# Optimization experiments

Measured on AMD Instinct MI355X. Metric: run time of the kernel, lower is better.

Reference implementation:

```python
import jax, jax.numpy as jnp
import numpy as np
import math

K_HEADS = 16  # nb_heads from init_kwargs


def setup_inputs() -> dict:
    key = jax.random.key(0)
    ks = jax.random.split(key, 7)
    B, M, H, D = 2, 2048, 1024, 1024 // K_HEADS
    return {
        "h": jax.random.normal(ks[0], (B, M, H), jnp.float32),
        "h_cache": jax.random.normal(ks[1], (B, M, H), jnp.float32),
        "key_pe": jax.random.normal(ks[2], (1, D, M), jnp.float32),
        "Wq": jax.random.normal(ks[3], (H, H), jnp.float32) * 0.02,
        "Wk": jax.random.normal(ks[4], (H, H), jnp.float32) * 0.02,
        "Wv": jax.random.normal(ks[5], (H, H), jnp.float32) * 0.02,
        "Wo": jax.random.normal(ks[6], (H, H), jnp.float32) * 0.02,
    }


def _heads(x, K):
    # [B, M, H] -> [B, K, M, D]
    B, M, H = x.shape
    return x.reshape(B, M, K, H // K).transpose(0, 2, 1, 3)


def reference(h, h_cache, key_pe, Wq, Wk, Wv, Wo):
    B, M, H = h.shape
    K = K_HEADS
    D = H // K
    q = _heads(h @ Wq.T, K)        # [B, K, M, D]
    k = _heads(h_cache @ Wk.T, K)  # [B, K, L, D], L == M
    v = _heads(h_cache @ Wv.T, K)  # [B, K, L, D]

    attn_cont = jnp.einsum("bkmd,bkld->bkml", q, k)            # content scores
    attn_pos = jnp.einsum("bkmd,dl->bkml", q, key_pe[0])       # positional scores
    attn = (attn_cont + attn_pos[..., :M]) / math.sqrt(D)
    attn = jax.nn.softmax(attn, axis=-1)  # computed as in source, but source
    # (faithfully) multiplies VALUE by attn_cont, not attn:
    out = jnp.einsum("bkml,bkld->bkmd", attn_cont, v)          # [B, K, M, D]
    out = out.transpose(0, 2, 1, 3).reshape(B, M, H)
    return out @ Wo.T
```

## Files before the change

kernel.cpp:

```cpp
#include <hip/hip_runtime.h>
#include <hip/hip_bf16.h>

#define BB 2
#define MM 2048
#define HH 1024
#define KH 16

typedef short s16x8 __attribute__((ext_vector_type(8)));
typedef float f32x4 __attribute__((ext_vector_type(4)));
typedef float f32x16 __attribute__((ext_vector_type(16)));

#define GLOBAL_AS __attribute__((address_space(1)))
#define LDS_AS    __attribute__((address_space(3)))

__device__ __forceinline__ void async_copy16(const void* g, void* l) {
    __builtin_amdgcn_global_load_lds((const GLOBAL_AS void*)g, (LDS_AS void*)l, 16, 0, 0);
}

struct __align__(8) bf16x4_t { __hip_bfloat16 x, y, z, w; };

__global__ __launch_bounds__(256) void cvt7(
    const float* __restrict__ s0, const float* __restrict__ s1,
    const float* __restrict__ s2, const float* __restrict__ s3,
    const float* __restrict__ s4, const float* __restrict__ s5,
    __hip_bfloat16* __restrict__ d0, __hip_bfloat16* __restrict__ d1,
    __hip_bfloat16* __restrict__ d2, __hip_bfloat16* __restrict__ d3,
    __hip_bfloat16* __restrict__ d4, __hip_bfloat16* __restrict__ d5,
    float* __restrict__ Sz)
{
    const int seg = blockIdx.y;
    const int i = (blockIdx.x * 256 + threadIdx.x) * 4;
    if (seg == 6) {
        if (i + 3 < BB * KH * 64 * 64) {
            float4 z = {0.f, 0.f, 0.f, 0.f};
            *(float4*)(Sz + i) = z;
        }
        return;
    }
    const float* src;
    __hip_bfloat16* dst;
    int n;
    switch (seg) {
        case 0: src = s0; dst = d0; n = BB * MM * HH; break;
        case 1: src = s1; dst = d1; n = BB * MM * HH; break;
        case 2: src = s2; dst = d2; n = HH * HH; break;
        case 3: src = s3; dst = d3; n = HH * HH; break;
        case 4: src = s4; dst = d4; n = HH * HH; break;
        default: src = s5; dst = d5; n = HH * HH; break;
    }
    if (i + 3 < n) {
        const float4 v = *(const float4*)(src + i);
        bf16x4_t o;
        o.x = __float2bfloat16(v.x);
        o.y = __float2bfloat16(v.y);
        o.z = __float2bfloat16(v.z);
        o.w = __float2bfloat16(v.w);
        *(bf16x4_t*)(dst + i) = o;
    }
}

__device__ __forceinline__ void store_c(__hip_bfloat16* C, size_t idx, float v) {
    C[idx] = __float2bfloat16(v);
}
__device__ __forceinline__ void store_c(float* C, size_t idx, float v) { C[idx] = v; }

template <typename OutT>
__device__ __forceinline__ void gemm_nt_body32(
    const __hip_bfloat16* __restrict__ A,
    const __hip_bfloat16* __restrict__ Bm,
    OutT* __restrict__ C,
    __hip_bfloat16* As, __hip_bfloat16* Bs,
    int m0, int n0)
{
    const int t    = threadIdx.x;
    const int lane = t & 63;
    const int wave = t >> 6;

    const int lr = lane >> 2;
    const int lc = (((lane & 3) ^ ((lane >> 3) & 3)) * 8);

    const int wm = (wave >> 1) * 64;
    const int wn = (wave & 1) * 64;
    const int fm = lane & 31;
    const int swr = (lane >> 1) & 3;
    const int ghi = lane >> 5;

    f32x16 acc[2][2] = {};

    for (int k0 = 0; k0 < HH; k0 += 32) {
        __syncthreads();
#pragma unroll
        for (int i = 0; i < 2; ++i) {
            const int c = wave * 2 + i;
            async_copy16(A  + (size_t)(m0 + c * 16 + lr) * HH + (k0 + lc), As + c * 512);
            async_copy16(Bm + (size_t)(n0 + c * 16 + lr) * HH + (k0 + lc), Bs + c * 512);
        }
        __syncthreads();

#pragma unroll
        for (int ks = 0; ks < 32; ks += 16) {
            const int pos = ((((ks >> 3) + ghi) ^ swr) * 8);
            s16x8 af[2], bf[2];
#pragma unroll
            for (int mi = 0; mi < 2; ++mi)
                af[mi] = *(const s16x8*)(As + (wm + mi * 32 + fm) * 32 + pos);
#pragma unroll
            for (int ni = 0; ni < 2; ++ni)
                bf[ni] = *(const s16x8*)(Bs + (wn + ni * 32 + fm) * 32 + pos);
#pragma unroll
            for (int mi = 0; mi < 2; ++mi)
#pragma unroll
                for (int ni = 0; ni < 2; ++ni)
                    acc[mi][ni] = __builtin_amdgcn_mfma_f32_32x32x16_bf16(
                        af[mi], bf[ni], acc[mi][ni], 0, 0, 0);
        }
    }

    const int ec = lane & 31;
    const int eb = (lane >> 5) * 4;
#pragma unroll
    for (int mi = 0; mi < 2; ++mi)
#pragma unroll
        for (int ni = 0; ni < 2; ++ni)
#pragma unroll
            for (int r = 0; r < 16; ++r) {
                const int m = m0 + wm + mi * 32 + (r & 3) + 8 * (r >> 2) + eb;
                const int n = n0 + wn + ni * 32 + ec;
                store_c(C, (size_t)m * HH + n, acc[mi][ni][r]);
            }
}

__global__ __launch_bounds__(256) void gemm_qkv(
    const __hip_bfloat16* __restrict__ hb,  const __hip_bfloat16* __restrict__ hcb,
    const __hip_bfloat16* __restrict__ wq,  const __hip_bfloat16* __restrict__ wk,
    const __hip_bfloat16* __restrict__ wv,
    __hip_bfloat16* __restrict__ Q, __hip_bfloat16* __restrict__ K,
    __hip_bfloat16* __restrict__ V)
{
    __shared__ __align__(16) __hip_bfloat16 As[128 * 32];
    __shared__ __align__(16) __hip_bfloat16 Bs[128 * 32];
    const int z = blockIdx.z;
    const __hip_bfloat16* A  = (z == 0) ? hb : hcb;
    const __hip_bfloat16* Bm = (z == 0) ? wq : (z == 1) ? wk : wv;
    __hip_bfloat16* C        = (z == 0) ? Q  : (z == 1) ? K  : V;
    gemm_nt_body32(A, Bm, C, As, Bs, blockIdx.x * 128, blockIdx.y * 128);
}

__global__ __launch_bounds__(256) void gemm_final(
    const __hip_bfloat16* __restrict__ Qg, const __hip_bfloat16* __restrict__ W2g,
    float* __restrict__ outg)
{
    __shared__ __align__(16) __hip_bfloat16 As[64 * 32];
    __shared__ __align__(16) __hip_bfloat16 Bs[128 * 32];

    const int b = blockIdx.z;
    const __hip_bfloat16* A  = Qg  + (size_t)b * MM * HH;
    const __hip_bfloat16* Bm = W2g + (size_t)b * HH * HH;
    float* C                 = outg + (size_t)b * MM * HH;
    const int m0 = blockIdx.x * 64;
    const int n0 = blockIdx.y * 128;

    const int t    = threadIdx.x;
    const int lane = t & 63;
    const int wave = t >> 6;
    const int lr = lane >> 2;
    const int lc = (((lane & 3) ^ ((lane >> 3) & 3)) * 8);
    const int fm = lane & 31;
    const int swr = (lane >> 1) & 3;
    const int ghi = lane >> 5;

    f32x16 acc[2] = {};

    for (int k0 = 0; k0 < HH; k0 += 32) {
        __syncthreads();
        async_copy16(A  + (size_t)(m0 + wave * 16 + lr) * HH + (k0 + lc),
                     As + wave * 512);
        async_copy16(Bm + (size_t)(n0 + (2 * wave) * 16 + lr) * HH + (k0 + lc),
                     Bs + (2 * wave) * 512);
        async_copy16(Bm + (size_t)(n0 + (2 * wave + 1) * 16 + lr) * HH + (k0 + lc),
                     Bs + (2 * wave + 1) * 512);
        __syncthreads();

#pragma unroll
        for (int ks = 0; ks < 32; ks += 16) {
            const int pos = ((((ks >> 3) + ghi) ^ swr) * 8);
            s16x8 af[2], bf;
#pragma unroll
            for (int mi = 0; mi < 2; ++mi)
                af[mi] = *(const s16x8*)(As + (mi * 32 + fm) * 32 + pos);
            bf = *(const s16x8*)(Bs + (wave * 32 + fm) * 32 + pos);
#pragma unroll
            for (int mi = 0; mi < 2; ++mi)
                acc[mi] = __builtin_amdgcn_mfma_f32_32x32x16_bf16(
                    af[mi], bf, acc[mi], 0, 0, 0);
        }
    }

    const int ec = lane & 31;
    const int eb = (lane >> 5) * 4;
#pragma unroll
    for (int mi = 0; mi < 2; ++mi)
#pragma unroll
        for (int r = 0; r < 16; ++r) {
            const int m = m0 + mi * 32 + (r & 3) + 8 * (r >> 2) + eb;
            const int n = n0 + wave * 32 + ec;
            C[(size_t)m * HH + n] = acc[mi][r];
        }
}

#define CH 128
#define LP 136

__global__ __launch_bounds__(256) void kv_outer_mfma(
    const __hip_bfloat16* __restrict__ Km,
    const __hip_bfloat16* __restrict__ Vm,
    float* __restrict__ S)
{
    __shared__ __align__(16) __hip_bfloat16 Kt[64 * LP];
    __shared__ __align__(16) __hip_bfloat16 Vt[64 * LP];

    const int t = threadIdx.x, head = blockIdx.y, b = blockIdx.z;
    const int l0 = blockIdx.x * CH;

    const int r  = t & 127;
    const int cb = (t >> 7) * 8;
    const size_t gbase = (size_t)(b * MM + l0 + r) * HH + head * 64;
#pragma unroll
    for (int u = 0; u < 4; ++u) {
        const int c8 = cb + u * 16;
        const s16x8 kv = *(const s16x8*)(Km + gbase + c8);
        const s16x8 vv = *(const s16x8*)(Vm + gbase + c8);
#pragma unroll
        for (int j = 0; j < 8; ++j) {
            Kt[(c8 + j) * LP + r] = ((const __hip_bfloat16*)&kv)[j];
            Vt[(c8 + j) * LP + r] = ((const __hip_bfloat16*)&vv)[j];
        }
    }
    __syncthreads();

    const int wave = t >> 6, lane = t & 63;
    const int fr = lane & 15;
    const int fq = (lane >> 4) * 8;
    const int wm = wave * 16;

    f32x4 acc[4] = {};
    for (int kk = 0; kk < CH; kk += 32) {
        const s16x8 af = *(const s16x8*)(Kt + (wm + fr) * LP + kk + fq);
        s16x8 bf[4];
#pragma unroll
        for (int nj = 0; nj < 4; ++nj)
            bf[nj] = *(const s16x8*)(Vt + (nj * 16 + fr) * LP + kk + fq);
#pragma unroll
        for (int nj = 0; nj < 4; ++nj)
            acc[nj] = __builtin_amdgcn_mfma_f32_16x16x32_bf16(af, bf[nj], acc[nj], 0, 0, 0);
    }

    float* Sg = S + ((size_t)b * KH + head) * 4096;
    const int er = (lane >> 4) * 4;
    const int ec = lane & 15;
#pragma unroll
    for (int nj = 0; nj < 4; ++nj)
#pragma unroll
        for (int rr = 0; rr < 4; ++rr)
            atomicAdd(&Sg[(wm + er + rr) * 64 + nj * 16 + ec], acc[nj][rr]);
}

__global__ __launch_bounds__(256) void w2_fold(
    const __hip_bfloat16* __restrict__ Wo,
    const float* __restrict__ S,
    __hip_bfloat16* __restrict__ W2)
{
    __shared__ float Sl[64 * 68];
    __shared__ float Wl[128 * 68];
    const int t = threadIdx.x, head = blockIdx.y, b = blockIdx.z;
    const int n0 = blockIdx.x * 128;

    const float* Sg = S + ((size_t)b * KH + head) * 4096;
    for (int idx = t; idx < 4096; idx += 256) {
        const int dp = idx >> 6, d = idx & 63;
        Sl[d * 68 + dp] = Sg[idx];
    }
    for (int idx = t; idx < 1024; idx += 256) {
        const int r = idx >> 3, c8 = (idx & 7) * 8;
        s16x8 wv = *(const s16x8*)(Wo + (size_t)(n0 + r) * HH + head * 64 + c8);
#pragma unroll
        for (int j = 0; j < 8; ++j) {
            __hip_bfloat16 wb = *(((const __hip_bfloat16*)&wv) + j);
            Wl[r * 68 + c8 + j] = __bfloat162float(wb);
        }
    }
    __syncthreads();

    const int dpb = (t & 15) * 4;
    const int ng  = t >> 4;
    float acc[8][4] = {};
    for (int d0 = 0; d0 < 64; d0 += 4) {
        f32x4 sv[4];
#pragma unroll
        for (int r = 0; r < 4; ++r)
            sv[r] = *(const f32x4*)(Sl + (d0 + r) * 68 + dpb);
#pragma unroll
        for (int i = 0; i < 8; ++i) {
            const f32x4 wv = *(const f32x4*)(Wl + (ng + 16 * i) * 68 + d0);
#pragma unroll
            for (int r = 0; r < 4; ++r)
#pragma unroll
                for (int j = 0; j < 4; ++j)
                    acc[i][j] += wv[r] * sv[r][j];
        }
    }

#pragma unroll
    for (int i = 0; i < 8; ++i) {
        bf16x4_t o;
        o.x = __float2bfloat16(acc[i][0]);
        o.y = __float2bfloat16(acc[i][1]);
        o.z = __float2bfloat16(acc[i][2]);
        o.w = __float2bfloat16(acc[i][3]);
        *(bf16x4_t*)(W2 + (size_t)b * HH * HH + (size_t)(n0 + ng + 16 * i) * HH
                     + head * 64 + dpb) = o;
    }
}

extern "C" void kernel_launch(void* const* d_in, const int* in_sizes, int n_in,
                              void* d_out, int out_size, void* d_ws, size_t ws_size,
                              hipStream_t stream) {
    const float* h_f  = (const float*)d_in[0];
    const float* hc_f = (const float*)d_in[1];
    const float* Wq_f = (const float*)d_in[3];
    const float* Wk_f = (const float*)d_in[4];
    const float* Wv_f = (const float*)d_in[5];
    const float* Wo_f = (const float*)d_in[6];
    float* out = (float*)d_out;

    const size_t act_b = (size_t)BB * MM * HH * 2;
    const size_t w_b   = (size_t)HH * HH * 2;
    char* ws = (char*)d_ws;
    __hip_bfloat16* hb   = (__hip_bfloat16*)(ws);
    __hip_bfloat16* hcb  = (__hip_bfloat16*)(ws + act_b);
    __hip_bfloat16* wqb  = (__hip_bfloat16*)(ws + 2 * act_b);
    __hip_bfloat16* wkb  = (__hip_bfloat16*)(ws + 2 * act_b + w_b);
    __hip_bfloat16* wvb  = (__hip_bfloat16*)(ws + 2 * act_b + 2 * w_b);
    __hip_bfloat16* wob  = (__hip_bfloat16*)(ws + 2 * act_b + 3 * w_b);
    __hip_bfloat16* Qbuf = (__hip_bfloat16*)(ws + 2 * act_b + 4 * w_b);
    __hip_bfloat16* Kbuf = (__hip_bfloat16*)(ws + 3 * act_b + 4 * w_b);
    __hip_bfloat16* Vbuf = (__hip_bfloat16*)(ws + 4 * act_b + 4 * w_b);
    float*          Sbuf = (float*)(ws + 5 * act_b + 4 * w_b);
    __hip_bfloat16* W2   = (__hip_bfloat16*)(ws + 5 * act_b + 4 * w_b + (size_t)512 * 1024);

    const dim3 blk(256);

    cvt7<<<dim3(4096, 7), blk, 0, stream>>>(h_f, hc_f, Wq_f, Wk_f, Wv_f, Wo_f,
                                            hb, hcb, wqb, wkb, wvb, wob, Sbuf);

    gemm_qkv<<<dim3(32, 8, 3), blk, 0, stream>>>(hb, hcb, wqb, wkb, wvb,
                                                 Qbuf, Kbuf, Vbuf);

    kv_outer_mfma<<<dim3(MM / CH, KH, BB), blk, 0, stream>>>(Kbuf, Vbuf, Sbuf);

    w2_fold<<<dim3(8, KH, BB), blk, 0, stream>>>(wob, Sbuf, W2);

    gemm_final<<<dim3(32, 8, 2), blk, 0, stream>>>(Qbuf, W2, out);
}
```

Baseline: 174.2 us.

## Fold Wq into per-batch output weight and drop the Q projection GEMM

```diff
diff --git a/kernel.cpp b/kernel.cpp
--- a/kernel.cpp
+++ b/kernel.cpp
@@ -19,18 +19,18 @@
 
 struct __align__(8) bf16x4_t { __hip_bfloat16 x, y, z, w; };
 
-__global__ __launch_bounds__(256) void cvt7(
+__global__ __launch_bounds__(256) void cvt6b(
     const float* __restrict__ s0, const float* __restrict__ s1,
     const float* __restrict__ s2, const float* __restrict__ s3,
-    const float* __restrict__ s4, const float* __restrict__ s5,
+    const float* __restrict__ s4,
     __hip_bfloat16* __restrict__ d0, __hip_bfloat16* __restrict__ d1,
     __hip_bfloat16* __restrict__ d2, __hip_bfloat16* __restrict__ d3,
-    __hip_bfloat16* __restrict__ d4, __hip_bfloat16* __restrict__ d5,
+    __hip_bfloat16* __restrict__ d4,
     float* __restrict__ Sz)
 {
     const int seg = blockIdx.y;
     const int i = (blockIdx.x * 256 + threadIdx.x) * 4;
-    if (seg == 6) {
+    if (seg == 5) {
         if (i + 3 < BB * KH * 64 * 64) {
             float4 z = {0.f, 0.f, 0.f, 0.f};
             *(float4*)(Sz + i) = z;
@@ -45,8 +45,7 @@
         case 1: src = s1; dst = d1; n = BB * MM * HH; break;
         case 2: src = s2; dst = d2; n = HH * HH; break;
         case 3: src = s3; dst = d3; n = HH * HH; break;
-        case 4: src = s4; dst = d4; n = HH * HH; break;
-        default: src = s5; dst = d5; n = HH * HH; break;
+        default: src = s4; dst = d4; n = HH * HH; break;
     }
     if (i + 3 < n) {
         const float4 v = *(const float4*)(src + i);
@@ -59,13 +58,31 @@
     }
 }
 
+__global__ __launch_bounds__(256) void transpose_wq(
+    const float* __restrict__ Wq, __hip_bfloat16* __restrict__ WqT)
+{
+    __shared__ float Tl[64][65];
+    const int j0 = blockIdx.x * 64;
+    const int k0 = blockIdx.y * 64;
+    const int t = threadIdx.x;
+    const int r = t >> 6;
+    const int c = t & 63;
+#pragma unroll
+    for (int i = 0; i < 64; i += 4)
+        Tl[r + i][c] = Wq[(size_t)(j0 + r + i) * HH + k0 + c];
+    __syncthreads();
+#pragma unroll
+    for (int i = 0; i < 64; i += 4)
+        WqT[(size_t)(k0 + r + i) * HH + j0 + c] = __float2bfloat16(Tl[c][r + i]);
+}
+
 __device__ __forceinline__ void store_c(__hip_bfloat16* C, size_t idx, float v) {
     C[idx] = __float2bfloat16(v);
 }
 __device__ __forceinline__ void store_c(float* C, size_t idx, float v) { C[idx] = v; }
 
 template <typename OutT>
-__device__ __forceinline__ void gemm_nt_body32(
+__device__ __forceinline__ void gemm_nt_body64(
     const __hip_bfloat16* __restrict__ A,
     const __hip_bfloat16* __restrict__ Bm,
     OutT* __restrict__ C,
@@ -76,37 +93,41 @@
     const int lane = t & 63;
     const int wave = t >> 6;
 
-    const int lr = lane >> 2;
-    const int lc = (((lane & 3) ^ ((lane >> 3) & 3)) * 8);
-
-    const int wm = (wave >> 1) * 64;
-    const int wn = (wave & 1) * 64;
-    const int fm = lane & 31;
-    const int swr = (lane >> 1) & 3;
+    const int srow = lane >> 3;
+    const int sw   = ((lane & 7) ^ srow) * 8;
+
+    const int wm  = (wave >> 1) * 64;
+    const int wn  = (wave & 1) * 64;
+    const int fm  = lane & 31;
+    const int fm7 = fm & 7;
     const int ghi = lane >> 5;
 
     f32x16 acc[2][2] = {};
 
-    for (int k0 = 0; k0 < HH; k0 += 32) {
+    for (int k0 = 0; k0 < HH; k0 += 64) {
         __syncthreads();
 #pragma unroll
         for (int i = 0; i < 2; ++i) {
             const int c = wave * 2 + i;
-            async_copy16(A  + (size_t)(m0 + c * 16 + lr) * HH + (k0 + lc), As + c * 512);
-            async_copy16(Bm + (size_t)(n0 + c * 16 + lr) * HH + (k0 + lc), Bs + c * 512);
+            const __hip_bfloat16* ag = A + (size_t)(m0 + c * 16 + srow) * HH + k0 + sw;
+            async_copy16(ag,          As + c * 1024);
+            async_copy16(ag + 8 * HH, As + c * 1024 + 512);
+            const __hip_bfloat16* bg = Bm + (size_t)(n0 + c * 16 + srow) * HH + k0 + sw;
+            async_copy16(bg,          Bs + c * 1024);
+            async_copy16(bg + 8 * HH, Bs + c * 1024 + 512);
         }
         __syncthreads();
 
 #pragma unroll
-        for (int ks = 0; ks < 32; ks += 16) {
-            const int pos = ((((ks >> 3) + ghi) ^ swr) * 8);
+        for (int ks = 0; ks < 64; ks += 16) {
+            const int pos = ((((ks >> 3) + ghi) ^ fm7) * 8);
             s16x8 af[2], bf[2];
 #pragma unroll
             for (int mi = 0; mi < 2; ++mi)
-                af[mi] = *(const s16x8*)(As + (wm + mi * 32 + fm) * 32 + pos);
+                af[mi] = *(const s16x8*)(As + (wm + mi * 32 + fm) * 64 + pos);
 #pragma unroll
             for (int ni = 0; ni < 2; ++ni)
-                bf[ni] = *(const s16x8*)(Bs + (wn + ni * 32 + fm) * 32 + pos);
+                bf[ni] = *(const s16x8*)(Bs + (wn + ni * 32 + fm) * 64 + pos);
 #pragma unroll
             for (int mi = 0; mi < 2; ++mi)
 #pragma unroll
@@ -130,65 +151,52 @@
             }
 }
 
-__global__ __launch_bounds__(256) void gemm_qkv(
-    const __hip_bfloat16* __restrict__ hb,  const __hip_bfloat16* __restrict__ hcb,
-    const __hip_bfloat16* __restrict__ wq,  const __hip_bfloat16* __restrict__ wk,
-    const __hip_bfloat16* __restrict__ wv,
-    __hip_bfloat16* __restrict__ Q, __hip_bfloat16* __restrict__ K,
-    __hip_bfloat16* __restrict__ V)
-{
-    __shared__ __align__(16) __hip_bfloat16 As[128 * 32];
-    __shared__ __align__(16) __hip_bfloat16 Bs[128 * 32];
-    const int z = blockIdx.z;
-    const __hip_bfloat16* A  = (z == 0) ? hb : hcb;
-    const __hip_bfloat16* Bm = (z == 0) ? wq : (z == 1) ? wk : wv;
-    __hip_bfloat16* C        = (z == 0) ? Q  : (z == 1) ? K  : V;
-    gemm_nt_body32(A, Bm, C, As, Bs, blockIdx.x * 128, blockIdx.y * 128);
-}
-
-__global__ __launch_bounds__(256) void gemm_final(
-    const __hip_bfloat16* __restrict__ Qg, const __hip_bfloat16* __restrict__ W2g,
-    float* __restrict__ outg)
-{
-    __shared__ __align__(16) __hip_bfloat16 As[64 * 32];
-    __shared__ __align__(16) __hip_bfloat16 Bs[128 * 32];
-
-    const int b = blockIdx.z;
-    const __hip_bfloat16* A  = Qg  + (size_t)b * MM * HH;
-    const __hip_bfloat16* Bm = W2g + (size_t)b * HH * HH;
-    float* C                 = outg + (size_t)b * MM * HH;
-    const int m0 = blockIdx.x * 64;
-    const int n0 = blockIdx.y * 128;
-
+template <typename OutT>
+__device__ __forceinline__ void gemm_nt_body64_m64(
+    const __hip_bfloat16* __restrict__ A,
+    const __hip_bfloat16* __restrict__ Bm,
+    OutT* __restrict__ C,
+    __hip_bfloat16* As, __hip_bfloat16* Bs,
+    int m0, int n0)
+{
     const int t    = threadIdx.x;
     const int lane = t & 63;
     const int wave = t >> 6;
-    const int lr = lane >> 2;
-    const int lc = (((lane & 3) ^ ((lane >> 3) & 3)) * 8);
-    const int fm = lane & 31;
-    const int swr = (lane >> 1) & 3;
+
+    const int srow = lane >> 3;
+    const int sw   = ((lane & 7) ^ srow) * 8;
+
+    const int wn  = wave * 32;
+    const int fm  = lane & 31;
+    const int fm7 = fm & 7;
     const int ghi = lane >> 5;
 
     f32x16 acc[2] = {};
 
-    for (int k0 = 0; k0 < HH; k0 += 32) {
+    for (int k0 = 0; k0 < HH; k0 += 64) {
         __syncthreads();
-        async_copy16(A  + (size_t)(m0 + wave * 16 + lr) * HH + (k0 + lc),
-                     As + wave * 512);
-        async_copy16(Bm + (size_t)(n0 + (2 * wave) * 16 + lr) * HH + (k0 + lc),
-                     Bs + (2 * wave) * 512);
-        async_copy16(Bm + (size_t)(n0 + (2 * wave + 1) * 16 + lr) * HH + (k0 + lc),
-                     Bs + (2 * wave + 1) * 512);
+        {
+            const __hip_bfloat16* ag = A + (size_t)(m0 + wave * 16 + srow) * HH + k0 + sw;
+            async_copy16(ag,          As + wave * 1024);
+            async_copy16(ag + 8 * HH, As + wave * 1024 + 512);
+        }
+#pragma unroll
+        for (int i = 0; i < 2; ++i) {
+            const int c = wave * 2 + i;
+            const __hip_bfloat16* bg = Bm + (size_t)(n0 + c * 16 + srow) * HH + k0 + sw;
+            async_copy16(bg,          Bs + c * 1024);
+            async_copy16(bg + 8 * HH, Bs + c * 1024 + 512);
+        }
         __syncthreads();
 
 #pragma unroll
-        for (int ks = 0; ks < 32; ks += 16) {
-            const int pos = ((((ks >> 3) + ghi) ^ swr) * 8);
+        for (int ks = 0; ks < 64; ks += 16) {
+            const int pos = ((((ks >> 3) + ghi) ^ fm7) * 8);
             s16x8 af[2], bf;
 #pragma unroll
             for (int mi = 0; mi < 2; ++mi)
-                af[mi] = *(const s16x8*)(As + (mi * 32 + fm) * 32 + pos);
-            bf = *(const s16x8*)(Bs + (wave * 32 + fm) * 32 + pos);
+                af[mi] = *(const s16x8*)(As + (mi * 32 + fm) * 64 + pos);
+            bf = *(const s16x8*)(Bs + (wn + fm) * 64 + pos);
 #pragma unroll
             for (int mi = 0; mi < 2; ++mi)
                 acc[mi] = __builtin_amdgcn_mfma_f32_32x32x16_bf16(
@@ -203,9 +211,44 @@
 #pragma unroll
         for (int r = 0; r < 16; ++r) {
             const int m = m0 + mi * 32 + (r & 3) + 8 * (r >> 2) + eb;
-            const int n = n0 + wave * 32 + ec;
-            C[(size_t)m * HH + n] = acc[mi][r];
-        }
+            const int n = n0 + wn + ec;
+            store_c(C, (size_t)m * HH + n, acc[mi][r]);
+        }
+}
+
+__global__ __launch_bounds__(256) void gemm_kv(
+    const __hip_bfloat16* __restrict__ hcb,
+    const __hip_bfloat16* __restrict__ wk, const __hip_bfloat16* __restrict__ wv,
+    __hip_bfloat16* __restrict__ K, __hip_bfloat16* __restrict__ V)
+{
+    __shared__ __align__(16) __hip_bfloat16 As[128 * 64];
+    __shared__ __align__(16) __hip_bfloat16 Bs[128 * 64];
+    const int z = blockIdx.z;
+    gemm_nt_body64(hcb, z ? wv : wk, z ? V : K, As, Bs,
+                   blockIdx.x * 128, blockIdx.y * 128);
+}
+
+__global__ __launch_bounds__(256) void gemm_f(
+    const __hip_bfloat16* __restrict__ W2, const __hip_bfloat16* __restrict__ WqT,
+    __hip_bfloat16* __restrict__ F)
+{
+    __shared__ __align__(16) __hip_bfloat16 As[64 * 64];
+    __shared__ __align__(16) __hip_bfloat16 Bs[128 * 64];
+    const int b = blockIdx.z;
+    gemm_nt_body64_m64(W2 + (size_t)b * HH * HH, WqT, F + (size_t)b * HH * HH,
+                       As, Bs, blockIdx.x * 64, blockIdx.y * 128);
+}
+
+__global__ __launch_bounds__(256) void gemm_final(
+    const __hip_bfloat16* __restrict__ hb, const __hip_bfloat16* __restrict__ F,
+    float* __restrict__ outg)
+{
+    __shared__ __align__(16) __hip_bfloat16 As[64 * 64];
+    __shared__ __align__(16) __hip_bfloat16 Bs[128 * 64];
+    const int b = blockIdx.z;
+    gemm_nt_body64_m64(hb + (size_t)b * MM * HH, F + (size_t)b * HH * HH,
+                       outg + (size_t)b * MM * HH, As, Bs,
+                       blockIdx.x * 64, blockIdx.y * 128);
 }
 
 #define CH 128
@@ -338,27 +381,29 @@
     char* ws = (char*)d_ws;
     __hip_bfloat16* hb   = (__hip_bfloat16*)(ws);
     __hip_bfloat16* hcb  = (__hip_bfloat16*)(ws + act_b);
-    __hip_bfloat16* wqb  = (__hip_bfloat16*)(ws + 2 * act_b);
-    __hip_bfloat16* wkb  = (__hip_bfloat16*)(ws + 2 * act_b + w_b);
-    __hip_bfloat16* wvb  = (__hip_bfloat16*)(ws + 2 * act_b + 2 * w_b);
-    __hip_bfloat16* wob  = (__hip_bfloat16*)(ws + 2 * act_b + 3 * w_b);
-    __hip_bfloat16* Qbuf = (__hip_bfloat16*)(ws + 2 * act_b + 4 * w_b);
-    __hip_bfloat16* Kbuf = (__hip_bfloat16*)(ws + 3 * act_b + 4 * w_b);
-    __hip_bfloat16* Vbuf = (__hip_bfloat16*)(ws + 4 * act_b + 4 * w_b);
-    float*          Sbuf = (float*)(ws + 5 * act_b + 4 * w_b);
-    __hip_bfloat16* W2   = (__hip_bfloat16*)(ws + 5 * act_b + 4 * w_b + (size_t)512 * 1024);
+    __hip_bfloat16* wkb  = (__hip_bfloat16*)(ws + 2 * act_b);
+    __hip_bfloat16* wvb  = (__hip_bfloat16*)(ws + 2 * act_b + w_b);
+    __hip_bfloat16* wob  = (__hip_bfloat16*)(ws + 2 * act_b + 2 * w_b);
+    __hip_bfloat16* wqt  = (__hip_bfloat16*)(ws + 2 * act_b + 3 * w_b);
+    __hip_bfloat16* Kbuf = (__hip_bfloat16*)(ws + 2 * act_b + 4 * w_b);
+    __hip_bfloat16* Vbuf = (__hip_bfloat16*)(ws + 3 * act_b + 4 * w_b);
+    float*          Sbuf = (float*)(ws + 4 * act_b + 4 * w_b);
+    __hip_bfloat16* W2   = (__hip_bfloat16*)(ws + 4 * act_b + 4 * w_b + (size_t)512 * 1024);
+    __hip_bfloat16* Fbuf = (__hip_bfloat16*)(ws + 4 * act_b + 6 * w_b + (size_t)512 * 1024);
 
     const dim3 blk(256);
 
-    cvt7<<<dim3(4096, 7), blk, 0, stream>>>(h_f, hc_f, Wq_f, Wk_f, Wv_f, Wo_f,
-                                            hb, hcb, wqb, wkb, wvb, wob, Sbuf);
-
-    gemm_qkv<<<dim3(32, 8, 3), blk, 0, stream>>>(hb, hcb, wqb, wkb, wvb,
-                                                 Qbuf, Kbuf, Vbuf);
+    cvt6b<<<dim3(4096, 6), blk, 0, stream>>>(h_f, hc_f, Wk_f, Wv_f, Wo_f,
+                                             hb, hcb, wkb, wvb, wob, Sbuf);
+    transpose_wq<<<dim3(16, 16), blk, 0, stream>>>(Wq_f, wqt);
+
+    gemm_kv<<<dim3(32, 8, 2), blk, 0, stream>>>(hcb, wkb, wvb, Kbuf, Vbuf);
 
     kv_outer_mfma<<<dim3(MM / CH, KH, BB), blk, 0, stream>>>(Kbuf, Vbuf, Sbuf);
 
     w2_fold<<<dim3(8, KH, BB), blk, 0, stream>>>(wob, Sbuf, W2);
 
-    gemm_final<<<dim3(32, 8, 2), blk, 0, stream>>>(Qbuf, W2, out);
-}
+    gemm_f<<<dim3(16, 8, 2), blk, 0, stream>>>(W2, wqt, Fbuf);
+
+    gemm_final<<<dim3(32, 8, 2), blk, 0, stream>>>(hb, Fbuf, out);
+}
```

Result: no change. 174.1 us (-0.1%).
